# Kernel optimization log

Hardware: AMD Instinct MI355X
Metric: run time of the kernel (lower is better)

The kernel has to match this reference:

```python
import jax, jax.numpy as jnp
from jax import lax
import numpy as np

B, T, CIN, COUT, H = 8, 128, 64, 64, 256


def setup_inputs() -> dict:
    key = jax.random.key(0)
    ks = jax.random.split(key, 8)
    return {
        "x": jax.random.normal(ks[0], (B, T, CIN, H, 1), dtype=jnp.float32),
        "h0": jax.random.uniform(ks[1], (B, COUT, H, 1), dtype=jnp.float32),
        "c0": jax.random.uniform(ks[2], (B, COUT, H, 1), dtype=jnp.float32),
        "conv_w": jax.random.normal(ks[3], (4 * COUT, CIN + COUT, 3), dtype=jnp.float32) * 0.05,
        "conv_b": jax.random.normal(ks[4], (4 * COUT,), dtype=jnp.float32) * 0.05,
        "Wci": jax.random.normal(ks[5], (1, COUT, H, 1), dtype=jnp.float32) * 0.02,
        "Wcf": jax.random.normal(ks[6], (1, COUT, H, 1), dtype=jnp.float32) * 0.02,
        "Wco": jax.random.normal(ks[7], (1, COUT, H, 1), dtype=jnp.float32) * 0.02,
    }


def _convlstm_scan(x, h0, c0, conv_w, conv_b, Wci, Wcf, Wco):
    # drop trailing width-1 dim; work in [B, C, H]
    x3 = x[..., 0]            # [B, T, Cin, H]
    h = h0[..., 0]            # [B, Cout, H]
    c = c0[..., 0]
    wci, wcf, wco = Wci[..., 0], Wcf[..., 0], Wco[..., 0]  # [1, Cout, H]
    b = conv_b[None, :, None]

    def step(carry, xt):
        h, c = carry
        cat = jnp.concatenate([xt, h], axis=1)  # [B, Cin+Cout, H]
        conv = lax.conv_general_dilated(
            cat, conv_w, window_strides=(1,), padding="SAME",
            dimension_numbers=("NCH", "OIH", "NCH")) + b  # [B, 4*Cout, H]
        i, f, g, o = jnp.split(conv, 4, axis=1)
        i = jax.nn.sigmoid(i + wci * c)
        f = jax.nn.sigmoid(f + wcf * c)
        c_new = f * c + i * jnp.tanh(g)
        o = jax.nn.sigmoid(o + wco * c_new)
        h_new = o * jnp.tanh(c_new)
        return (h_new, c_new), (h_new, c_new)

    (_, _), (hs, cs) = lax.scan(step, (h, c), jnp.swapaxes(x3, 0, 1))
    # hs, cs: [T, B, Cout, H] -> [B, T, Cout, H, 1]
    hs = jnp.swapaxes(hs, 0, 1)[..., None]
    cs = jnp.swapaxes(cs, 0, 1)[..., None]
    return hs, cs


def reference(x, h0, c0, conv_w, conv_b, Wci, Wcf, Wco):
    return _convlstm_scan(x, h0, c0, conv_w, conv_b, Wci, Wcf, Wco)
```

## Files before the change

### kernel.cpp

```cpp
#include <hip/hip_runtime.h>


constexpr int Bn    = 8;
constexpr int Tn    = 128;
constexpr int CINn  = 64;
constexpr int COUTn = 64;
constexpr int Hn    = 256;
constexpr int ICAT  = CINn + COUTn;
constexpr int PP    = 64;

__device__ __forceinline__ float sigmoidf_(float v) {
    return 1.0f / (1.0f + __expf(-v));
}

__global__ __launch_bounds__(256) void convlstm_step(
    const float* __restrict__ x,
    const float* __restrict__ h0,
    const float* __restrict__ c0,
    const float* __restrict__ wg,
    const float* __restrict__ bias,
    const float* __restrict__ wci,
    const float* __restrict__ wcf,
    const float* __restrict__ wco,
    float* __restrict__ hs,
    float* __restrict__ cs,
    int t)
{
    __shared__ float cat[66 * 128];
    __shared__ float conv_out[32 * 64];

    const int tid = threadIdx.x;
    const int p_l = tid & 63;
    const int icg = tid >> 6;
    const int p0  = blockIdx.x * PP;
    const int b   = blockIdx.y;
    const int coz = blockIdx.z;

    const float* xt = x + (size_t)(b * Tn + t) * CINn * Hn;
    const float* hp = (t == 0) ? (h0 + (size_t)b * COUTn * Hn)
                               : (hs + (size_t)(b * Tn + (t - 1)) * COUTn * Hn);
    const float* cp = (t == 0) ? (c0 + (size_t)b * COUTn * Hn)
                               : (cs + (size_t)(b * Tn + (t - 1)) * COUTn * Hn);

    {
        float vals[32];
#pragma unroll
        for (int icc = 0; icc < 32; ++icc) {
            const int ic = icc * 4 + icg;
            const float* src = (ic < CINn) ? (xt + (size_t)ic * Hn)
                                           : (hp + (size_t)(ic - CINn) * Hn);
            vals[icc] = src[p0 + p_l];
        }
        const int row = p_l + 1;
#pragma unroll
        for (int icc = 0; icc < 32; ++icc) {
            const int ic   = icc * 4 + icg;
            const int slot = (ic >> 2) ^ (row & 31);
            cat[row * 128 + slot * 4 + (ic & 3)] = vals[icc];
        }
        if (tid < 128) {
            const int ic = tid;
            float v = 0.0f;
            if (p0 > 0) {
                const float* src = (ic < CINn) ? (xt + (size_t)ic * Hn)
                                               : (hp + (size_t)(ic - CINn) * Hn);
                v = src[p0 - 1];
            }
            const int slot = (ic >> 2);
            cat[slot * 4 + (ic & 3)] = v;
        } else {
            const int ic = tid - 128;
            float v = 0.0f;
            if (p0 + PP < Hn) {
                const float* src = (ic < CINn) ? (xt + (size_t)ic * Hn)
                                               : (hp + (size_t)(ic - CINn) * Hn);
                v = src[p0 + PP];
            }
            const int slot = (ic >> 2) ^ (65 & 31);
            cat[65 * 128 + slot * 4 + (ic & 3)] = v;
        }
    }
    __syncthreads();

    const int wv    = __builtin_amdgcn_readfirstlane(tid >> 6);
    const int chan0 = wv * COUTn + coz * 8;
    const float* wbase = wg + (size_t)chan0 * (ICAT * 3);

    float acc[8];
#pragma unroll
    for (int k = 0; k < 8; ++k) acc[k] = bias[chan0 + k];

    const float4* cat4 = (const float4*)cat;
    const int r0 = p_l, r1 = p_l + 1, r2 = p_l + 2;
    const int s0 = (r0 & 31), s1 = (r1 & 31), s2 = (r2 & 31);

#pragma unroll 2
    for (int icq = 0; icq < 32; ++icq) {
        const float4 a0 = cat4[r0 * 32 + (icq ^ s0)];
        const float4 a1 = cat4[r1 * 32 + (icq ^ s1)];
        const float4 a2 = cat4[r2 * 32 + (icq ^ s2)];
        const float in0[4] = {a0.x, a0.y, a0.z, a0.w};
        const float in1[4] = {a1.x, a1.y, a1.z, a1.w};
        const float in2[4] = {a2.x, a2.y, a2.z, a2.w};
#pragma unroll
        for (int k = 0; k < 8; ++k) {
            const float* wr = wbase + (size_t)k * (ICAT * 3) + icq * 12;
#pragma unroll
            for (int i = 0; i < 4; ++i) {
                acc[k] = fmaf(wr[3 * i + 0], in0[i],
                          fmaf(wr[3 * i + 1], in1[i],
                          fmaf(wr[3 * i + 2], in2[i], acc[k])));
            }
        }
    }

#pragma unroll
    for (int k = 0; k < 8; ++k)
        conv_out[(wv * 8 + k) * 64 + p_l] = acc[k];
    __syncthreads();

    const int c2 = tid >> 6;
    const int pg = p0 + p_l;
#pragma unroll
    for (int j = 0; j < 2; ++j) {
        const int co_l = c2 * 2 + j;
        const int co   = coz * 8 + co_l;
        const float pi = conv_out[(0 * 8 + co_l) * 64 + p_l];
        const float pf = conv_out[(1 * 8 + co_l) * 64 + p_l];
        const float pg_ = conv_out[(2 * 8 + co_l) * 64 + p_l];
        const float po = conv_out[(3 * 8 + co_l) * 64 + p_l];

        const size_t cidx = (size_t)co * Hn + pg;
        const float cprev = cp[cidx];
        const float iv = sigmoidf_(pi + wci[cidx] * cprev);
        const float fv = sigmoidf_(pf + wcf[cidx] * cprev);
        const float gv = tanhf(pg_);
        const float cn = fv * cprev + iv * gv;
        const float ov = sigmoidf_(po + wco[cidx] * cn);
        const float hn = ov * tanhf(cn);

        const size_t oidx = ((size_t)(b * Tn + t) * COUTn + co) * Hn + pg;
        hs[oidx] = hn;
        cs[oidx] = cn;
    }
}

extern "C" void kernel_launch(void* const* d_in, const int* in_sizes, int n_in,
                              void* d_out, int out_size, void* d_ws, size_t ws_size,
                              hipStream_t stream) {
    (void)in_sizes; (void)n_in; (void)out_size; (void)d_ws; (void)ws_size;

    const float* x    = (const float*)d_in[0];
    const float* h0   = (const float*)d_in[1];
    const float* c0   = (const float*)d_in[2];
    const float* w    = (const float*)d_in[3];
    const float* bias = (const float*)d_in[4];
    const float* wci  = (const float*)d_in[5];
    const float* wcf  = (const float*)d_in[6];
    const float* wco  = (const float*)d_in[7];

    float* hs = (float*)d_out;
    float* cs = hs + (size_t)Bn * Tn * COUTn * Hn;

    dim3 grid(Hn / PP, Bn, 8);
    for (int t = 0; t < Tn; ++t) {
        convlstm_step<<<grid, 256, 0, stream>>>(
            x, h0, c0, w, bias, wci, wcf, wco, hs, cs, t);
    }
}
```

Measured before the change: 2.853 ms.

## Replace per-timestep launches with a persistent cooperative kernel using grid sync

Turns the 128 per-timestep kernel launches into one cooperative launch of 256 blocks that loops over time and calls grid.sync between steps. Each block stages its slice of the conv weights in LDS once and keeps the cell state and peephole weights in registers, so they are not reloaded from global memory every step. This removes launch overhead and the repeated weight and state traffic. In exchange it adds a grid-wide barrier per step and needs all 256 blocks to be co-resident, with roughly 85KB of LDS per block.

```diff
diff --git a/kernel.cpp b/kernel.cpp
--- a/kernel.cpp
+++ b/kernel.cpp
@@ -1,4 +1,7 @@
 #include <hip/hip_runtime.h>
+#include <hip/hip_cooperative_groups.h>
+
+namespace cg = cooperative_groups;
 
 
 constexpr int Bn    = 8;
@@ -13,7 +16,7 @@
     return 1.0f / (1.0f + __expf(-v));
 }
 
-__global__ __launch_bounds__(256) void convlstm_step(
+__global__ __launch_bounds__(256, 1) void convlstm_persist(
     const float* __restrict__ x,
     const float* __restrict__ h0,
     const float* __restrict__ c0,
@@ -23,125 +26,167 @@
     const float* __restrict__ wcf,
     const float* __restrict__ wco,
     float* __restrict__ hs,
-    float* __restrict__ cs,
-    int t)
+    float* __restrict__ cs)
 {
+    __shared__ float wlds[32 * 384];
     __shared__ float cat[66 * 128];
     __shared__ float conv_out[32 * 64];
 
     const int tid = threadIdx.x;
+    const int blk = blockIdx.x;
+    const int coz = (blk >> 3) & 7;
+    const int gid = ((blk >> 6) << 3) + (blk & 7);
+    const int b   = gid >> 2;
+    const int p0  = (gid & 3) * PP;
+
     const int p_l = tid & 63;
     const int icg = tid >> 6;
-    const int p0  = blockIdx.x * PP;
-    const int b   = blockIdx.y;
-    const int coz = blockIdx.z;
-
-    const float* xt = x + (size_t)(b * Tn + t) * CINn * Hn;
-    const float* hp = (t == 0) ? (h0 + (size_t)b * COUTn * Hn)
-                               : (hs + (size_t)(b * Tn + (t - 1)) * COUTn * Hn);
-    const float* cp = (t == 0) ? (c0 + (size_t)b * COUTn * Hn)
-                               : (cs + (size_t)(b * Tn + (t - 1)) * COUTn * Hn);
-
-    {
-        float vals[32];
-#pragma unroll
-        for (int icc = 0; icc < 32; ++icc) {
-            const int ic = icc * 4 + icg;
-            const float* src = (ic < CINn) ? (xt + (size_t)ic * Hn)
-                                           : (hp + (size_t)(ic - CINn) * Hn);
-            vals[icc] = src[p0 + p_l];
+    const int wv  = __builtin_amdgcn_readfirstlane(tid >> 6);
+
+    for (int f = tid; f < 32 * 384; f += 256) {
+        const int lr = f / 384;
+        const int j  = f - lr * 384;
+        const int grow = (lr >> 3) * COUTn + coz * 8 + (lr & 7);
+        wlds[f] = wg[(size_t)grow * (ICAT * 3) + j];
+    }
+
+    float bias_r[8];
+#pragma unroll
+    for (int k = 0; k < 8; ++k)
+        bias_r[k] = bias[wv * COUTn + coz * 8 + k];
+
+    const int pg = p0 + p_l;
+    float c_reg[2], wci_r[2], wcf_r[2], wco_r[2];
+#pragma unroll
+    for (int j = 0; j < 2; ++j) {
+        const int co = coz * 8 + wv * 2 + j;
+        const size_t cidx = (size_t)co * Hn + pg;
+        wci_r[j] = wci[cidx];
+        wcf_r[j] = wcf[cidx];
+        wco_r[j] = wco[cidx];
+        c_reg[j] = c0[(size_t)b * COUTn * Hn + cidx];
+    }
+
+    cg::grid_group grid = cg::this_grid();
+
+    for (int t = 0; t < Tn; ++t) {
+        const float* xt = x + (size_t)(b * Tn + t) * CINn * Hn;
+        const float* hp = (t == 0)
+            ? (h0 + (size_t)b * COUTn * Hn)
+            : (hs + (size_t)(b * Tn + (t - 1)) * COUTn * Hn);
+
+        {
+            float vx[16], vh[16];
+#pragma unroll
+            for (int icc = 0; icc < 16; ++icc)
+                vx[icc] = xt[(size_t)(icc * 4 + icg) * Hn + pg];
+#pragma unroll
+            for (int icc = 0; icc < 16; ++icc)
+                vh[icc] = hp[(size_t)(icc * 4 + icg) * Hn + pg];
+
+            const int row = p_l + 1;
+#pragma unroll
+            for (int icc = 0; icc < 16; ++icc) {
+                const int ic   = icc * 4 + icg;
+                const int slot = (ic >> 2) ^ (row & 31);
+                cat[row * 128 + slot * 4 + (ic & 3)] = vx[icc];
+            }
+#pragma unroll
+            for (int icc = 0; icc < 16; ++icc) {
+                const int ic   = (icc + 16) * 4 + icg;
+                const int slot = (ic >> 2) ^ (row & 31);
+                cat[row * 128 + slot * 4 + (ic & 3)] = vh[icc];
+            }
+            if (tid < 128) {
+                const int ic = tid;
+                float v = 0.0f;
+                if (p0 > 0) {
+                    const float* src = (ic < CINn)
+                        ? (xt + (size_t)ic * Hn)
+                        : (hp + (size_t)(ic - CINn) * Hn);
+                    v = src[p0 - 1];
+                }
+                cat[(ic >> 2) * 4 + (ic & 3)] = v;
+            } else {
+                const int ic = tid - 128;
+                float v = 0.0f;
+                if (p0 + PP < Hn) {
+                    const float* src = (ic < CINn)
+                        ? (xt + (size_t)ic * Hn)
+                        : (hp + (size_t)(ic - CINn) * Hn);
+                    v = src[p0 + PP];
+                }
+                const int slot = (ic >> 2) ^ 1;
+                cat[65 * 128 + slot * 4 + (ic & 3)] = v;
+            }
         }
-        const int row = p_l + 1;
-#pragma unroll
-        for (int icc = 0; icc < 32; ++icc) {
-            const int ic   = icc * 4 + icg;
-            const int slot = (ic >> 2) ^ (row & 31);
-            cat[row * 128 + slot * 4 + (ic & 3)] = vals[icc];
+        __syncthreads();
+
+        float acc[8];
+#pragma unroll
+        for (int k = 0; k < 8; ++k) acc[k] = bias_r[k];
+
+        const float4* cat4 = (const float4*)cat;
+        const float4* w4   = (const float4*)wlds;
+        const int r0 = p_l, r1 = p_l + 1, r2 = p_l + 2;
+        const int s0 = r0 & 31, s1 = r1 & 31, s2 = r2 & 31;
+
+#pragma unroll 2
+        for (int icq = 0; icq < 32; ++icq) {
+            const float4 a0 = cat4[r0 * 32 + (icq ^ s0)];
+            const float4 a1 = cat4[r1 * 32 + (icq ^ s1)];
+            const float4 a2 = cat4[r2 * 32 + (icq ^ s2)];
+            const float in0[4] = {a0.x, a0.y, a0.z, a0.w};
+            const float in1[4] = {a1.x, a1.y, a1.z, a1.w};
+            const float in2[4] = {a2.x, a2.y, a2.z, a2.w};
+#pragma unroll
+            for (int k = 0; k < 8; ++k) {
+                const int base = (((wv * 8 + k) * 384 + icq * 12) >> 2);
+                const float4 w0 = w4[base];
+                const float4 w1 = w4[base + 1];
+                const float4 w2 = w4[base + 2];
+                const float wr_[12] = {w0.x, w0.y, w0.z, w0.w,
+                                       w1.x, w1.y, w1.z, w1.w,
+                                       w2.x, w2.y, w2.z, w2.w};
+#pragma unroll
+                for (int i = 0; i < 4; ++i) {
+                    acc[k] = fmaf(wr_[3 * i + 0], in0[i],
+                              fmaf(wr_[3 * i + 1], in1[i],
+                              fmaf(wr_[3 * i + 2], in2[i], acc[k])));
+                }
+            }
         }
-        if (tid < 128) {
-            const int ic = tid;
-            float v = 0.0f;
-            if (p0 > 0) {
-                const float* src = (ic < CINn) ? (xt + (size_t)ic * Hn)
-                                               : (hp + (size_t)(ic - CINn) * Hn);
-                v = src[p0 - 1];
-            }
-            const int slot = (ic >> 2);
-            cat[slot * 4 + (ic & 3)] = v;
-        } else {
-            const int ic = tid - 128;
-            float v = 0.0f;
-            if (p0 + PP < Hn) {
-                const float* src = (ic < CINn) ? (xt + (size_t)ic * Hn)
-                                               : (hp + (size_t)(ic - CINn) * Hn);
-                v = src[p0 + PP];
-            }
-            const int slot = (ic >> 2) ^ (65 & 31);
-            cat[65 * 128 + slot * 4 + (ic & 3)] = v;
+
+#pragma unroll
+        for (int k = 0; k < 8; ++k)
+            conv_out[(wv * 8 + k) * 64 + p_l] = acc[k];
+        __syncthreads();
+
+#pragma unroll
+        for (int j = 0; j < 2; ++j) {
+            const int co_l = wv * 2 + j;
+            const float pi  = conv_out[(0 * 8 + co_l) * 64 + p_l];
+            const float pf  = conv_out[(1 * 8 + co_l) * 64 + p_l];
+            const float pgg = conv_out[(2 * 8 + co_l) * 64 + p_l];
+            const float po  = conv_out[(3 * 8 + co_l) * 64 + p_l];
+
+            const float cprev = c_reg[j];
+            const float iv = sigmoidf_(pi + wci_r[j] * cprev);
+            const float fv = sigmoidf_(pf + wcf_r[j] * cprev);
+            const float gv = tanhf(pgg);
+            const float cn = fv * cprev + iv * gv;
+            const float ov = sigmoidf_(po + wco_r[j] * cn);
+            const float hn = ov * tanhf(cn);
+            c_reg[j] = cn;
+
+            const int co = coz * 8 + co_l;
+            const size_t oidx = ((size_t)(b * Tn + t) * COUTn + co) * Hn + pg;
+            hs[oidx] = hn;
+            cs[oidx] = cn;
         }
-    }
-    __syncthreads();
-
-    const int wv    = __builtin_amdgcn_readfirstlane(tid >> 6);
-    const int chan0 = wv * COUTn + coz * 8;
-    const float* wbase = wg + (size_t)chan0 * (ICAT * 3);
-
-    float acc[8];
-#pragma unroll
-    for (int k = 0; k < 8; ++k) acc[k] = bias[chan0 + k];
-
-    const float4* cat4 = (const float4*)cat;
-    const int r0 = p_l, r1 = p_l + 1, r2 = p_l + 2;
-    const int s0 = (r0 & 31), s1 = (r1 & 31), s2 = (r2 & 31);
-
-#pragma unroll 2
-    for (int icq = 0; icq < 32; ++icq) {
-        const float4 a0 = cat4[r0 * 32 + (icq ^ s0)];
-        const float4 a1 = cat4[r1 * 32 + (icq ^ s1)];
-        const float4 a2 = cat4[r2 * 32 + (icq ^ s2)];
-        const float in0[4] = {a0.x, a0.y, a0.z, a0.w};
-        const float in1[4] = {a1.x, a1.y, a1.z, a1.w};
-        const float in2[4] = {a2.x, a2.y, a2.z, a2.w};
-#pragma unroll
-        for (int k = 0; k < 8; ++k) {
-            const float* wr = wbase + (size_t)k * (ICAT * 3) + icq * 12;
-#pragma unroll
-            for (int i = 0; i < 4; ++i) {
-                acc[k] = fmaf(wr[3 * i + 0], in0[i],
-                          fmaf(wr[3 * i + 1], in1[i],
-                          fmaf(wr[3 * i + 2], in2[i], acc[k])));
-            }
-        }
-    }
-
-#pragma unroll
-    for (int k = 0; k < 8; ++k)
-        conv_out[(wv * 8 + k) * 64 + p_l] = acc[k];
-    __syncthreads();
-
-    const int c2 = tid >> 6;
-    const int pg = p0 + p_l;
-#pragma unroll
-    for (int j = 0; j < 2; ++j) {
-        const int co_l = c2 * 2 + j;
-        const int co   = coz * 8 + co_l;
-        const float pi = conv_out[(0 * 8 + co_l) * 64 + p_l];
-        const float pf = conv_out[(1 * 8 + co_l) * 64 + p_l];
-        const float pg_ = conv_out[(2 * 8 + co_l) * 64 + p_l];
-        const float po = conv_out[(3 * 8 + co_l) * 64 + p_l];
-
-        const size_t cidx = (size_t)co * Hn + pg;
-        const float cprev = cp[cidx];
-        const float iv = sigmoidf_(pi + wci[cidx] * cprev);
-        const float fv = sigmoidf_(pf + wcf[cidx] * cprev);
-        const float gv = tanhf(pg_);
-        const float cn = fv * cprev + iv * gv;
-        const float ov = sigmoidf_(po + wco[cidx] * cn);
-        const float hn = ov * tanhf(cn);
-
-        const size_t oidx = ((size_t)(b * Tn + t) * COUTn + co) * Hn + pg;
-        hs[oidx] = hn;
-        cs[oidx] = cn;
+
+        __threadfence();
+        grid.sync();
     }
 }
 
@@ -162,9 +207,9 @@
     float* hs = (float*)d_out;
     float* cs = hs + (size_t)Bn * Tn * COUTn * Hn;
 
-    dim3 grid(Hn / PP, Bn, 8);
-    for (int t = 0; t < Tn; ++t) {
-        convlstm_step<<<grid, 256, 0, stream>>>(
-            x, h0, c0, w, bias, wci, wcf, wco, hs, cs, t);
-    }
+    void* args[] = {(void*)&x, (void*)&h0, (void*)&c0, (void*)&w,
+                    (void*)&bias, (void*)&wci, (void*)&wcf, (void*)&wco,
+                    (void*)&hs, (void*)&cs};
+    hipLaunchCooperativeKernel((const void*)convlstm_persist,
+                               dim3(256), dim3(256), args, 0, stream);
 }
```

After: 9.151 ms. +220.8%, slower.
